# Kernel optimization log

Measured on AMD Instinct MI355X. Metric: run time of the kernel, lower is better.

## Reference

```python
import jax, jax.numpy as jnp
import numpy as np
import math

ATTN_DIM = 16
TAU = 1.0
B, N = 4, 4096


def setup_inputs() -> dict:
    key = jax.random.key(0)
    k_x, k_q, k_k, k_v, k_o = jax.random.split(key, 5)
    return {
        "x": jax.random.normal(k_x, (B, N), dtype=jnp.float32),
        "w_q": jax.random.normal(k_q, (1, ATTN_DIM), dtype=jnp.float32),
        "w_k": jax.random.normal(k_k, (1, ATTN_DIM), dtype=jnp.float32),
        "w_v": jax.random.normal(k_v, (1, ATTN_DIM), dtype=jnp.float32),
        "w_out": jax.random.normal(k_o, (ATTN_DIM,), dtype=jnp.float32),
    }


def reference(x, w_q, w_k, w_v, w_out):
    # x: [B, N] scalar tokens -> outer products with small learned vectors
    x_tokens = x[..., None]                      # [B, N, 1]
    q = x_tokens * w_q                           # [B, N, D]
    k = x_tokens * w_k                           # [B, N, D]
    v = x_tokens * w_v                           # [B, N, D]
    scale = 1.0 / math.sqrt(ATTN_DIM)
    scores = jnp.einsum('bnd,bmd->bnm', q, k) * scale   # [B, N, N]
    weights = jax.nn.softmax(scores / TAU, axis=-1)     # [B, N, N]
    attn = jnp.einsum('bnm,bmd->bnd', weights, v)       # [B, N, D]
    return jnp.einsum('bnd,d->bn', attn, w_out)         # [B, N]
```

## Files before the change

kernel.cpp:

```cpp
#include <hip/hip_runtime.h>
#include <math.h>

#define BATCH 4
#define NTOK 4096
#define ATTN_D 16
#define BLOCK 256
#define ROWS_PER_WAVE 4
#define ROWS_PER_BLOCK 16
#define CHUNKS_PER_BATCH (NTOK / ROWS_PER_BLOCK)
#define GRID (BATCH * CHUNKS_PER_BATCH)

__global__ __launch_bounds__(BLOCK) void attn_collapsed_kernel(
    const float* __restrict__ x,
    const float* __restrict__ wq,
    const float* __restrict__ wk,
    const float* __restrict__ wv,
    const float* __restrict__ wout,
    float* __restrict__ out)
{
    __shared__ float sx[NTOK];
    __shared__ float sred[8];

    const int tid  = threadIdx.x;
    const int lane = tid & 63;
    const int wave = tid >> 6;
    const int b     = blockIdx.x >> 8;
    const int chunk = blockIdx.x & 255;

    const float* xb = x + b * NTOK;

    float vmax = -INFINITY, vmin = INFINITY;
    const float4* x4 = (const float4*)xb;
    float4* s4 = (float4*)sx;
    #pragma unroll
    for (int i = 0; i < NTOK / 4 / BLOCK; ++i) {
        float4 v = x4[tid + i * BLOCK];
        s4[tid + i * BLOCK] = v;
        vmax = fmaxf(vmax, fmaxf(fmaxf(v.x, v.y), fmaxf(v.z, v.w)));
        vmin = fminf(vmin, fminf(fminf(v.x, v.y), fminf(v.z, v.w)));
    }
    #pragma unroll
    for (int off = 32; off > 0; off >>= 1) {
        vmax = fmaxf(vmax, __shfl_xor(vmax, off));
        vmin = fminf(vmin, __shfl_xor(vmin, off));
    }
    if (lane == 0) { sred[wave] = vmax; sred[4 + wave] = vmin; }
    __syncthreads();
    vmax = fmaxf(fmaxf(sred[0], sred[1]), fmaxf(sred[2], sred[3]));
    vmin = fminf(fminf(sred[4], sred[5]), fminf(sred[6], sred[7]));

    float cqk = 0.f, cvo = 0.f;
    #pragma unroll
    for (int d = 0; d < ATTN_D; ++d) {
        cqk = fmaf(wq[d], wk[d], cqk);
        cvo = fmaf(wv[d], wout[d], cvo);
    }

    const float LOG2E = 1.4426950408889634f;
    const int row0 = chunk * ROWS_PER_BLOCK + wave * ROWS_PER_WAVE;

    float a2[ROWS_PER_WAVE], M2[ROWS_PER_WAVE];
    float S0[ROWS_PER_WAVE], S1[ROWS_PER_WAVE];
    #pragma unroll
    for (int r = 0; r < ROWS_PER_WAVE; ++r) {
        float xr = sx[row0 + r];
        float an = 0.25f * cqk * xr;
        float Mn = (an >= 0.f) ? an * vmax : an * vmin;
        a2[r] = an * LOG2E;
        M2[r] = Mn * LOG2E;
        S0[r] = 0.f;
        S1[r] = 0.f;
    }

    #pragma unroll 4
    for (int i = 0; i < NTOK / 4 / 64; ++i) {
        float4 xm4 = s4[lane + i * 64];
        #pragma unroll
        for (int c = 0; c < 4; ++c) {
            float xm = (c == 0) ? xm4.x : (c == 1) ? xm4.y : (c == 2) ? xm4.z : xm4.w;
            #pragma unroll
            for (int r = 0; r < ROWS_PER_WAVE; ++r) {
                float e = __builtin_amdgcn_exp2f(fmaf(a2[r], xm, -M2[r]));
                S0[r] += e;
                S1[r] = fmaf(xm, e, S1[r]);
            }
        }
    }

    #pragma unroll
    for (int r = 0; r < ROWS_PER_WAVE; ++r) {
        float s0 = S0[r], s1 = S1[r];
        #pragma unroll
        for (int off = 32; off > 0; off >>= 1) {
            s0 += __shfl_xor(s0, off);
            s1 += __shfl_xor(s1, off);
        }
        if (lane == 0) out[b * NTOK + row0 + r] = cvo * (s1 / s0);
    }
}

extern "C" void kernel_launch(void* const* d_in, const int* in_sizes, int n_in,
                              void* d_out, int out_size, void* d_ws, size_t ws_size,
                              hipStream_t stream) {
    const float* x    = (const float*)d_in[0];
    const float* wq   = (const float*)d_in[1];
    const float* wk   = (const float*)d_in[2];
    const float* wv   = (const float*)d_in[3];
    const float* wout = (const float*)d_in[4];
    float* out = (float*)d_out;

    attn_collapsed_kernel<<<dim3(GRID), dim3(BLOCK), 0, stream>>>(
        x, wq, wk, wv, wout, out);
}
```

Measured before the change: 70.67 us.

## Approximate per-row softmax ratio with Chebyshev interpolation over 64 nodes

Instead of evaluating the exact O(N^2) exp sums for every query row, the kernel evaluates the smooth function f(a)=sum x e^{a x}/sum e^{a x} at 64 Chebyshev nodes spanning the range of query coefficients. It then builds Chebyshev coefficients and evaluates each row's output with a Clenshaw recurrence. This cuts the exponential work from N*N to 64*N per batch and launches only one block per batch. It trades exactness for an approximation whose accuracy depends on the input range and the fixed node count, and it uses only 4 blocks on the GPU.

```diff
diff --git a/kernel.cpp b/kernel.cpp
--- a/kernel.cpp
+++ b/kernel.cpp
@@ -4,13 +4,12 @@
 #define BATCH 4
 #define NTOK 4096
 #define ATTN_D 16
-#define BLOCK 256
-#define ROWS_PER_WAVE 4
-#define ROWS_PER_BLOCK 16
-#define CHUNKS_PER_BATCH (NTOK / ROWS_PER_BLOCK)
-#define GRID (BATCH * CHUNKS_PER_BATCH)
+#define KNODES 64
+#define BLOCK 1024
+#define NWAVES (BLOCK / 64)
+#define M_PER_WAVE (NTOK / NWAVES)
 
-__global__ __launch_bounds__(BLOCK) void attn_collapsed_kernel(
+__global__ __launch_bounds__(BLOCK) void attn_cheb_kernel(
     const float* __restrict__ x,
     const float* __restrict__ wq,
     const float* __restrict__ wk,
@@ -19,35 +18,34 @@
     float* __restrict__ out)
 {
     __shared__ float sx[NTOK];
-    __shared__ float sred[8];
+    __shared__ float psum[NWAVES][KNODES][2];
+    __shared__ float sred[2 * NWAVES];
+    __shared__ float cx[KNODES];
 
     const int tid  = threadIdx.x;
     const int lane = tid & 63;
     const int wave = tid >> 6;
-    const int b     = blockIdx.x >> 8;
-    const int chunk = blockIdx.x & 255;
+    const int b    = blockIdx.x;
 
     const float* xb = x + b * NTOK;
 
-    float vmax = -INFINITY, vmin = INFINITY;
-    const float4* x4 = (const float4*)xb;
-    float4* s4 = (float4*)sx;
-    #pragma unroll
-    for (int i = 0; i < NTOK / 4 / BLOCK; ++i) {
-        float4 v = x4[tid + i * BLOCK];
-        s4[tid + i * BLOCK] = v;
-        vmax = fmaxf(vmax, fmaxf(fmaxf(v.x, v.y), fmaxf(v.z, v.w)));
-        vmin = fminf(vmin, fminf(fminf(v.x, v.y), fminf(v.z, v.w)));
-    }
+    float4 v = ((const float4*)xb)[tid];
+    ((float4*)sx)[tid] = v;
+    float vmax = fmaxf(fmaxf(v.x, v.y), fmaxf(v.z, v.w));
+    float vmin = fminf(fminf(v.x, v.y), fminf(v.z, v.w));
     #pragma unroll
     for (int off = 32; off > 0; off >>= 1) {
         vmax = fmaxf(vmax, __shfl_xor(vmax, off));
         vmin = fminf(vmin, __shfl_xor(vmin, off));
     }
-    if (lane == 0) { sred[wave] = vmax; sred[4 + wave] = vmin; }
+    if (lane == 0) { sred[wave] = vmax; sred[NWAVES + wave] = vmin; }
     __syncthreads();
-    vmax = fmaxf(fmaxf(sred[0], sred[1]), fmaxf(sred[2], sred[3]));
-    vmin = fminf(fminf(sred[4], sred[5]), fminf(sred[6], sred[7]));
+    vmax = sred[0]; vmin = sred[NWAVES];
+    #pragma unroll
+    for (int w = 1; w < NWAVES; ++w) {
+        vmax = fmaxf(vmax, sred[w]);
+        vmin = fminf(vmin, sred[NWAVES + w]);
+    }
 
     float cqk = 0.f, cvo = 0.f;
     #pragma unroll
@@ -56,47 +54,85 @@
         cvo = fmaf(wv[d], wout[d], cvo);
     }
 
-    const float LOG2E = 1.4426950408889634f;
-    const int row0 = chunk * ROWS_PER_BLOCK + wave * ROWS_PER_WAVE;
+    const float s   = 0.25f * cqk;
+    const float alo = fminf(s * vmin, s * vmax);
+    const float ahi = fmaxf(s * vmin, s * vmax);
+    const float ctr = 0.5f * (alo + ahi);
+    const float hw  = fmaxf(0.5f * (ahi - alo), 1e-30f);
 
-    float a2[ROWS_PER_WAVE], M2[ROWS_PER_WAVE];
-    float S0[ROWS_PER_WAVE], S1[ROWS_PER_WAVE];
-    #pragma unroll
-    for (int r = 0; r < ROWS_PER_WAVE; ++r) {
-        float xr = sx[row0 + r];
-        float an = 0.25f * cqk * xr;
-        float Mn = (an >= 0.f) ? an * vmax : an * vmin;
-        a2[r] = an * LOG2E;
-        M2[r] = Mn * LOG2E;
-        S0[r] = 0.f;
-        S1[r] = 0.f;
-    }
+    const float PI_OVER = 3.14159265358979323846f / (2.0f * KNODES);
+    const float LOG2E   = 1.4426950408889634f;
 
+    const float an = fmaf(hw, cosf((float)(2 * lane + 1) * PI_OVER), ctr);
+    const float a2 = an * LOG2E;
+    const float M2 = ((an >= 0.f) ? an * vmax : an * vmin) * LOG2E;
+
+    float S0 = 0.f, S1 = 0.f;
+    const float4* s4 = (const float4*)sx;
     #pragma unroll 4
-    for (int i = 0; i < NTOK / 4 / 64; ++i) {
-        float4 xm4 = s4[lane + i * 64];
+    for (int i = 0; i < M_PER_WAVE / 4; ++i) {
+        float4 xm4 = s4[wave * (M_PER_WAVE / 4) + i];
         #pragma unroll
         for (int c = 0; c < 4; ++c) {
             float xm = (c == 0) ? xm4.x : (c == 1) ? xm4.y : (c == 2) ? xm4.z : xm4.w;
-            #pragma unroll
-            for (int r = 0; r < ROWS_PER_WAVE; ++r) {
-                float e = __builtin_amdgcn_exp2f(fmaf(a2[r], xm, -M2[r]));
-                S0[r] += e;
-                S1[r] = fmaf(xm, e, S1[r]);
-            }
+            float e = __builtin_amdgcn_exp2f(fmaf(a2, xm, -M2));
+            S0 += e;
+            S1 = fmaf(xm, e, S1);
         }
     }
+    psum[wave][lane][0] = S0;
+    psum[wave][lane][1] = S1;
+    __syncthreads();
 
+    if (wave == 0) {
+        float t0 = 0.f, t1 = 0.f;
+        #pragma unroll
+        for (int w = 0; w < NWAVES; ++w) {
+            t0 += psum[w][lane][0];
+            t1 += psum[w][lane][1];
+        }
+        psum[0][lane][0] = t1 / t0;
+    }
+    __syncthreads();
+
+    if (wave == 0) {
+        double acc = 0.0;
+        for (int j = 0; j < KNODES; ++j) {
+            int u = ((2 * j + 1) * lane) & (4 * KNODES - 1);
+            acc += (double)(psum[0][j][0] * cosf((float)u * PI_OVER));
+        }
+        cx[lane] = (float)(acc * (2.0 / (double)KNODES));
+    }
+    __syncthreads();
+
+    const float ihw = 1.0f / hw;
+    float4 xr = s4[tid];
+    float tt[4], t2[4];
     #pragma unroll
-    for (int r = 0; r < ROWS_PER_WAVE; ++r) {
-        float s0 = S0[r], s1 = S1[r];
+    for (int i = 0; i < 4; ++i) {
+        float xi = (i == 0) ? xr.x : (i == 1) ? xr.y : (i == 2) ? xr.z : xr.w;
+        tt[i] = fmaf(s, xi, -ctr) * ihw;
+        t2[i] = 2.0f * tt[i];
+    }
+    float b1v[4] = {0.f, 0.f, 0.f, 0.f};
+    float b2v[4] = {0.f, 0.f, 0.f, 0.f};
+    for (int k = KNODES - 1; k >= 1; --k) {
+        float ck = cx[k];
         #pragma unroll
-        for (int off = 32; off > 0; off >>= 1) {
-            s0 += __shfl_xor(s0, off);
-            s1 += __shfl_xor(s1, off);
+        for (int i = 0; i < 4; ++i) {
+            float b0 = fmaf(t2[i], b1v[i], ck - b2v[i]);
+            b2v[i] = b1v[i];
+            b1v[i] = b0;
         }
-        if (lane == 0) out[b * NTOK + row0 + r] = cvo * (s1 / s0);
     }
+    const float c0h = 0.5f * cx[0];
+    float4 o;
+    float* op = &o.x;
+    #pragma unroll
+    for (int i = 0; i < 4; ++i) {
+        op[i] = cvo * fmaf(tt[i], b1v[i], c0h - b2v[i]);
+    }
+    ((float4*)(out + b * NTOK))[tid] = o;
 }
 
 extern "C" void kernel_launch(void* const* d_in, const int* in_sizes, int n_in,
@@ -109,6 +145,6 @@
     const float* wout = (const float*)d_in[4];
     float* out = (float*)d_out;
 
-    attn_collapsed_kernel<<<dim3(GRID), dim3(BLOCK), 0, stream>>>(
+    attn_cheb_kernel<<<dim3(BATCH), dim3(BLOCK), 0, stream>>>(
         x, wq, wk, wv, wout, out);
 }
```

Result: slower. 79.47 us (+12.5%).
